# Kernel tuning notes

Measured on AMD Instinct MI355X. Metric: run time of the kernel, lower is better.

The kernel has to match this reference:

```python
import jax, jax.numpy as jnp
import numpy as np

N_NODES = 50000
N_EDGES = 600000
IN_SIZE = 128
HIDDEN = 256
OUT_SIZE = 128


def _xavier(key, shape):
    fan_out, fan_in = shape
    lim = jnp.sqrt(6.0 / (fan_in + fan_out))
    return jax.random.uniform(key, shape, jnp.float32, -lim, lim)


def setup_inputs() -> dict:
    key = jax.random.key(0)
    ks = jax.random.split(key, 8)
    feat = jax.random.normal(ks[0], (N_NODES, IN_SIZE), jnp.float32)
    edge_index = jax.random.randint(ks[1], (2, N_EDGES), 0, N_NODES, jnp.int32)
    return {
        "feat": feat,
        "edge_index": edge_index,
        "W1l": _xavier(ks[2], (HIDDEN, IN_SIZE)),
        "b1": jnp.zeros((HIDDEN,), jnp.float32),
        "W1r": _xavier(ks[3], (HIDDEN, IN_SIZE)),
        "W2l": _xavier(ks[4], (OUT_SIZE, HIDDEN)),
        "b2": jnp.zeros((OUT_SIZE,), jnp.float32),
        "W2r": _xavier(ks[5], (OUT_SIZE, HIDDEN)),
        "Wfc": _xavier(ks[6], (2, OUT_SIZE)),
        "bfc": jnp.zeros((2,), jnp.float32),
    }


def _sage_conv(x, src, dst, Wl, bl, Wr):
    # mean-aggregate neighbor features: messages x[src] scattered to dst
    agg = jax.ops.segment_sum(x[src], dst, num_segments=N_NODES)
    cnt = jax.ops.segment_sum(jnp.ones((src.shape[0],), x.dtype), dst,
                              num_segments=N_NODES)
    agg = agg / jnp.maximum(cnt, 1.0)[:, None]
    out = agg @ Wl.T + bl + x @ Wr.T
    # F.normalize(p=2, dim=-1), eps=1e-12
    norm = jnp.maximum(jnp.linalg.norm(out, axis=-1, keepdims=True), 1e-12)
    return out / norm


def reference(feat, edge_index, W1l, b1, W1r, W2l, b2, W2r, Wfc, bfc):
    src, dst = edge_index[0], edge_index[1]
    h = _sage_conv(feat, src, dst, W1l, b1, W1r)
    h = jax.nn.relu(h)
    h = _sage_conv(h, src, dst, W2l, b2, W2r)
    logits = h @ Wfc.T + bfc
    return jax.nn.softmax(logits, axis=-1)
```

## Files before the change

### kernel.cpp

```cpp
#include <hip/hip_runtime.h>
#include <hip/hip_fp8.h>
#include <math.h>

#define N_NODES  50000
#define N_EDGES  600000
#define CAP      64
#define NB_ZERO  ((N_NODES + 255) / 256)

typedef __attribute__((ext_vector_type(8))) short bf16x8;
typedef __attribute__((ext_vector_type(4))) float f32x4;
typedef unsigned int uint32;

__device__ __forceinline__ unsigned short f2bf(float x) {
  uint32 u = __builtin_bit_cast(uint32, x);
  u += 0x7FFFu + ((u >> 16) & 1u);
  return (unsigned short)(u >> 16);
}
__device__ __forceinline__ float bf2f(uint32 lo16) {
  return __builtin_bit_cast(float, lo16 << 16);
}
__device__ __forceinline__ uint32 pack2(float a, float b) {
  return (uint32)f2bf(a) | ((uint32)f2bf(b) << 16);
}
__device__ __forceinline__ unsigned char f2q(float x) {
  __hip_fp8_e4m3 q(x);
  return __builtin_bit_cast(unsigned char, q);
}
__device__ __forceinline__ float q2f(uint32 b) {
  return (float)__builtin_bit_cast(__hip_fp8_e4m3, (unsigned char)(b & 0xffu));
}

#define PREP_FEAT_BLOCKS 12500
#define PREP_W_BLOCKS    256
__global__ void k_prep(const float* __restrict__ feat, unsigned short* __restrict__ featb,
                       unsigned short* __restrict__ feat8,
                       const float* __restrict__ W1l, const float* __restrict__ W1r,
                       unsigned short* __restrict__ Wc1,
                       const float* __restrict__ W2l, const float* __restrict__ W2r,
                       unsigned short* __restrict__ Wc2,
                       int* __restrict__ cnt) {
  const int bid = blockIdx.x, t = threadIdx.x;
  if (bid < PREP_FEAT_BLOCKS) {
    int i = bid * 256 + t;
    float2 v = ((const float2*)feat)[i];
    ((uint32*)featb)[i] = pack2(v.x, v.y);
    feat8[i] = (unsigned short)f2q(v.x) | ((unsigned short)f2q(v.y) << 8);
  } else if (bid < PREP_FEAT_BLOCKS + PREP_W_BLOCKS) {
    int id = (bid - PREP_FEAT_BLOCKS) * 256 + t;
    int n = id >> 8, k = id & 255;
    float v = (k < 128) ? W1l[n * 128 + k] : W1r[n * 128 + (k - 128)];
    Wc1[id] = f2bf(v);
  } else if (bid < PREP_FEAT_BLOCKS + 2 * PREP_W_BLOCKS) {
    int id = (bid - PREP_FEAT_BLOCKS - PREP_W_BLOCKS) * 256 + t;
    int n = id >> 8, k = id & 255;
    float v = (n < 128) ? W2l[n * 256 + k] : W2r[(n - 128) * 256 + k];
    Wc2[id] = f2bf(v);
  } else {
    int i = (bid - PREP_FEAT_BLOCKS - 2 * PREP_W_BLOCKS) * 256 + t;
    if (i < N_NODES) cnt[i] = 0;
  }
}
#define PREP_BLOCKS (PREP_FEAT_BLOCKS + 2 * PREP_W_BLOCKS + NB_ZERO)

__global__ void k_fill(const int* __restrict__ src, const int* __restrict__ dst,
                       int* __restrict__ cnt, int* __restrict__ col) {
  int i = blockIdx.x * 256 + threadIdx.x;
  if (i < N_EDGES) {
    int d = dst[i];
    int p = atomicAdd(&cnt[d], 1);
    if (p < CAP) col[(size_t)d * CAP + p] = src[i];
  }
}

__device__ __forceinline__ void gather8f8(const uint32* __restrict__ base,
                                          const int* __restrict__ col,
                                          int rs, int dg, int sl, float4& out) {
  int idx[8];
  #pragma unroll
  for (int q = 0; q < 8; ++q) idx[q] = col[rs + q];
  float4 a[8];
  #pragma unroll
  for (int q = 0; q < 8; ++q) a[q] = (float4){0.f, 0.f, 0.f, 0.f};
  int j = 0;
  for (; j + 8 <= dg; j += 8) {
    uint32 v[8];
    #pragma unroll
    for (int q = 0; q < 8; ++q) v[q] = base[(size_t)idx[q] * 32 + sl];
    #pragma unroll
    for (int q = 0; q < 8; ++q) idx[q] = col[rs + j + 8 + q];
    #pragma unroll
    for (int q = 0; q < 8; ++q) {
      a[q].x += q2f(v[q]);
      a[q].y += q2f(v[q] >> 8);
      a[q].z += q2f(v[q] >> 16);
      a[q].w += q2f(v[q] >> 24);
    }
  }
  #pragma unroll
  for (int q = 0; q < 7; ++q) {
    if (j + q < dg) {
      uint32 v = base[(size_t)idx[q] * 32 + sl];
      a[q].x += q2f(v);
      a[q].y += q2f(v >> 8);
      a[q].z += q2f(v >> 16);
      a[q].w += q2f(v >> 24);
    }
  }
  float4 s01, s23, s45, s67, s03, s47;
  s01.x = a[0].x + a[1].x; s01.y = a[0].y + a[1].y; s01.z = a[0].z + a[1].z; s01.w = a[0].w + a[1].w;
  s23.x = a[2].x + a[3].x; s23.y = a[2].y + a[3].y; s23.z = a[2].z + a[3].z; s23.w = a[2].w + a[3].w;
  s45.x = a[4].x + a[5].x; s45.y = a[4].y + a[5].y; s45.z = a[4].z + a[5].z; s45.w = a[4].w + a[5].w;
  s67.x = a[6].x + a[7].x; s67.y = a[6].y + a[7].y; s67.z = a[6].z + a[7].z; s67.w = a[6].w + a[7].w;
  s03.x = s01.x + s23.x; s03.y = s01.y + s23.y; s03.z = s01.z + s23.z; s03.w = s01.w + s23.w;
  s47.x = s45.x + s67.x; s47.y = s45.y + s67.y; s47.z = s45.z + s67.z; s47.w = s45.w + s67.w;
  out.x = s03.x + s47.x; out.y = s03.y + s47.y; out.z = s03.z + s47.z; out.w = s03.w + s47.w;
}

__global__ void k_agg1(const unsigned short* __restrict__ feat8, const int* __restrict__ cnt,
                       const int* __restrict__ col, unsigned short* __restrict__ agg) {
  int lane = threadIdx.x & 63;
  int half = lane >> 5, sl = lane & 31;
  int n = blockIdx.x * 8 + (threadIdx.x >> 6) * 2 + half;
  int dg = min(cnt[n], CAP);
  float4 s;
  gather8f8((const uint32*)feat8, col, n * CAP, dg, sl, s);
  float inv = 1.0f / fmaxf((float)dg, 1.0f);
  uint2 o;
  o.x = pack2(s.x * inv, s.y * inv);
  o.y = pack2(s.z * inv, s.w * inv);
  ((uint2*)agg)[(size_t)n * 32 + sl] = o;
}

__global__ __launch_bounds__(256, 3) void k_gemm1(
    const unsigned short* __restrict__ A0, const unsigned short* __restrict__ A1,
    const unsigned short* __restrict__ W, const float* __restrict__ bias,
    unsigned short* __restrict__ Y) {
  __shared__ unsigned short Ws[2048 * 8];
  __shared__ float red[4][32];
  const int t = threadIdx.x, lane = t & 63, w = t >> 6;
  const int mi = lane & 15, quad = lane >> 4;
  const int rowHalf = w >> 1, colHalf = w & 1;
  const int m0 = blockIdx.x * 64 + rowHalf * 32;
  const int col0 = colHalf * 128;
  const int rowA0 = min(m0 + mi, N_NODES - 1);
  const int rowA1 = min(m0 + 16 + mi, N_NODES - 1);

  f32x4 acc[2][8];
  #pragma unroll
  for (int rt = 0; rt < 2; ++rt)
    #pragma unroll
    for (int nt = 0; nt < 8; ++nt) acc[rt][nt] = (f32x4){0.f, 0.f, 0.f, 0.f};

  #pragma unroll
  for (int ks = 0; ks < 4; ++ks) {
    if (ks) __syncthreads();
    #pragma unroll
    for (int i = 0; i < 8; ++i) {
      int ch0 = (w * 8 + i) * 64;
      int qp = ch0 >> 8, n0 = ch0 & 255;
      const unsigned short* gp = W + (size_t)(n0 + lane) * 256 + ks * 64 + qp * 8;
      unsigned short* lp = Ws + (size_t)ch0 * 8;
      __builtin_amdgcn_global_load_lds(
          (const __attribute__((address_space(1))) void*)gp,
          (__attribute__((address_space(3))) void*)lp, 16, 0, 0);
    }
    const unsigned short* Asrc = (ks < 2) ? A0 : A1;
    const int koff = (ks & 1) * 64;
    bf16x8 af[2][2];
    af[0][0] = *(const bf16x8*)(Asrc + (size_t)rowA0 * 128 + koff + quad * 8);
    af[0][1] = *(const bf16x8*)(Asrc + (size_t)rowA0 * 128 + koff + 32 + quad * 8);
    af[1][0] = *(const bf16x8*)(Asrc + (size_t)rowA1 * 128 + koff + quad * 8);
    af[1][1] = *(const bf16x8*)(Asrc + (size_t)rowA1 * 128 + koff + 32 + quad * 8);
    __syncthreads();
    #pragma unroll
    for (int kc = 0; kc < 2; ++kc)
      #pragma unroll
      for (int nt = 0; nt < 8; ++nt) {
        bf16x8 b = *(const bf16x8*)(Ws + ((size_t)(kc * 4 + quad) * 256 + col0 + nt * 16 + mi) * 8);
        acc[0][nt] = __builtin_amdgcn_mfma_f32_16x16x32_bf16(af[0][kc], b, acc[0][nt], 0, 0, 0);
        acc[1][nt] = __builtin_amdgcn_mfma_f32_16x16x32_bf16(af[1][kc], b, acc[1][nt], 0, 0, 0);
      }
  }

  float ss[2][4] = {};
  #pragma unroll
  for (int nt = 0; nt < 8; ++nt) {
    float bv = bias[col0 + nt * 16 + mi];
    #pragma unroll
    for (int rt = 0; rt < 2; ++rt)
      #pragma unroll
      for (int r = 0; r < 4; ++r) {
        float v = acc[rt][nt][r] + bv;
        acc[rt][nt][r] = v;
        ss[rt][r] += v * v;
      }
  }
  #pragma unroll
  for (int rt = 0; rt < 2; ++rt)
    #pragma unroll
    for (int r = 0; r < 4; ++r) {
      float s = ss[rt][r];
      s += __shfl_xor(s, 1, 64);
      s += __shfl_xor(s, 2, 64);
      s += __shfl_xor(s, 4, 64);
      s += __shfl_xor(s, 8, 64);
      ss[rt][r] = s;
    }
  __syncthreads();
  if (mi == 0) {
    #pragma unroll
    for (int rt = 0; rt < 2; ++rt)
      #pragma unroll
      for (int r = 0; r < 4; ++r)
        red[w][rt * 16 + quad * 4 + r] = ss[rt][r];
  }
  __syncthreads();
  #pragma unroll
  for (int rt = 0; rt < 2; ++rt)
    #pragma unroll
    for (int r = 0; r < 4; ++r) {
      float full = ss[rt][r] + red[w ^ 1][rt * 16 + quad * 4 + r];
      ss[rt][r] = 1.0f / fmaxf(sqrtf(full), 1e-12f);
    }
  #pragma unroll
  for (int rt = 0; rt < 2; ++rt)
    #pragma unroll
    for (int r = 0; r < 4; ++r) {
      int row = m0 + rt * 16 + quad * 4 + r;
      if (row < N_NODES) {
        #pragma unroll
        for (int nt = 0; nt < 8; ++nt)
          Y[(size_t)row * 256 + col0 + nt * 16 + mi] =
              f2bf(fmaxf(acc[rt][nt][r] * ss[rt][r], 0.f));
      }
    }
}

__global__ __launch_bounds__(256, 3) void k_gemm2(
    const unsigned short* __restrict__ A0, const unsigned short* __restrict__ A1,
    const unsigned short* __restrict__ W,
    unsigned char* __restrict__ Tl8, unsigned short* __restrict__ Yr) {
  __shared__ unsigned short Ws[2048 * 8];
  const int t = threadIdx.x, lane = t & 63, w = t >> 6;
  const int mi = lane & 15, quad = lane >> 4;
  const int rb = blockIdx.x >> 1, chh = blockIdx.x & 1;
  const int m0 = rb * 128 + w * 32;
  const int col0 = chh * 128;
  const int rowA0 = min(m0 + mi, N_NODES - 1);
  const int rowA1 = min(m0 + 16 + mi, N_NODES - 1);

  f32x4 acc[2][8];
  #pragma unroll
  for (int rt = 0; rt < 2; ++rt)
    #pragma unroll
    for (int nt = 0; nt < 8; ++nt) acc[rt][nt] = (f32x4){0.f, 0.f, 0.f, 0.f};

  #pragma unroll
  for (int ks = 0; ks < 2; ++ks) {
    if (ks) __syncthreads();
    #pragma unroll
    for (int i = 0; i < 8; ++i) {
      int ch0 = (w * 8 + i) * 64;
      int qp = ch0 >> 7, n0 = ch0 & 127;
      const unsigned short* gp = W + (size_t)(col0 + n0 + lane) * 256 + ks * 128 + qp * 8;
      unsigned short* lp = Ws + (size_t)ch0 * 8;
      __builtin_amdgcn_global_load_lds(
          (const __attribute__((address_space(1))) void*)gp,
          (__attribute__((address_space(3))) void*)lp, 16, 0, 0);
    }
    const unsigned short* Asrc = ks ? A1 : A0;
    bf16x8 af[2][4];
    #pragma unroll
    for (int c = 0; c < 4; ++c) {
      af[0][c] = *(const bf16x8*)(Asrc + (size_t)rowA0 * 256 + c * 32 + quad * 8);
      af[1][c] = *(const bf16x8*)(Asrc + (size_t)rowA1 * 256 + c * 32 + quad * 8);
    }
    __syncthreads();
    #pragma unroll
    for (int c = 0; c < 4; ++c)
      #pragma unroll
      for (int nt = 0; nt < 8; ++nt) {
        bf16x8 b = *(const bf16x8*)(Ws + ((size_t)(c * 4 + quad) * 128 + nt * 16 + mi) * 8);
        acc[0][nt] = __builtin_amdgcn_mfma_f32_16x16x32_bf16(af[0][c], b, acc[0][nt], 0, 0, 0);
        acc[1][nt] = __builtin_amdgcn_mfma_f32_16x16x32_bf16(af[1][c], b, acc[1][nt], 0, 0, 0);
      }
  }

  if (chh == 0) {
    #pragma unroll
    for (int rt = 0; rt < 2; ++rt)
      #pragma unroll
      for (int r = 0; r < 4; ++r) {
        int row = m0 + rt * 16 + quad * 4 + r;
        if (row < N_NODES) {
          #pragma unroll
          for (int nt = 0; nt < 8; ++nt)
            Tl8[(size_t)row * 128 + nt * 16 + mi] = f2q(acc[rt][nt][r]);
        }
      }
  } else {
    #pragma unroll
    for (int rt = 0; rt < 2; ++rt)
      #pragma unroll
      for (int r = 0; r < 4; ++r) {
        int row = m0 + rt * 16 + quad * 4 + r;
        if (row < N_NODES) {
          #pragma unroll
          for (int nt = 0; nt < 8; ++nt)
            Yr[(size_t)row * 128 + nt * 16 + mi] = f2bf(acc[rt][nt][r]);
        }
      }
  }
}

__global__ void k_final(const unsigned char* __restrict__ Tl8, const unsigned short* __restrict__ Tr,
                        const int* __restrict__ cnt, const int* __restrict__ col,
                        const float* __restrict__ b2, const float* __restrict__ Wfc,
                        const float* __restrict__ bfc, float* __restrict__ out) {
  int lane = threadIdx.x & 63;
  int half = lane >> 5, sl = lane & 31;
  int n = blockIdx.x * 8 + (threadIdx.x >> 6) * 2 + half;
  int dg = min(cnt[n], CAP);
  uint2 tv = ((const uint2*)Tr)[(size_t)n * 32 + sl];
  float4 bb = ((const float4*)b2)[sl];
  float4 w0 = ((const float4*)Wfc)[sl];
  float4 w1 = ((const float4*)Wfc)[32 + sl];
  float4 s;
  gather8f8((const uint32*)Tl8, col, n * CAP, dg, sl, s);
  float inv = 1.0f / fmaxf((float)dg, 1.0f);
  float h0 = s.x * inv + bf2f(tv.x & 0xffffu) + bb.x;
  float h1 = s.y * inv + bf2f(tv.x >> 16) + bb.y;
  float h2 = s.z * inv + bf2f(tv.y & 0xffffu) + bb.z;
  float h3 = s.w * inv + bf2f(tv.y >> 16) + bb.w;
  float ss = h0 * h0 + h1 * h1 + h2 * h2 + h3 * h3;
  ss += __shfl_xor(ss, 1, 64);
  ss += __shfl_xor(ss, 2, 64);
  ss += __shfl_xor(ss, 4, 64);
  ss += __shfl_xor(ss, 8, 64);
  ss += __shfl_xor(ss, 16, 64);
  float iv = 1.0f / fmaxf(sqrtf(ss), 1e-12f);
  h0 *= iv; h1 *= iv; h2 *= iv; h3 *= iv;
  float p0 = h0 * w0.x + h1 * w0.y + h2 * w0.z + h3 * w0.w;
  float p1 = h0 * w1.x + h1 * w1.y + h2 * w1.z + h3 * w1.w;
  #pragma unroll
  for (int m = 1; m < 32; m <<= 1) {
    p0 += __shfl_xor(p0, m, 64);
    p1 += __shfl_xor(p1, m, 64);
  }
  if (sl == 0) {
    float l0 = p0 + bfc[0], l1 = p1 + bfc[1];
    float mx = fmaxf(l0, l1);
    float e0 = expf(l0 - mx), e1 = expf(l1 - mx);
    float sden = 1.0f / (e0 + e1);
    out[(size_t)n * 2 + 0] = e0 * sden;
    out[(size_t)n * 2 + 1] = e1 * sden;
  }
}

extern "C" void kernel_launch(void* const* d_in, const int* in_sizes, int n_in,
                              void* d_out, int out_size, void* d_ws, size_t ws_size,
                              hipStream_t stream) {
  const float* feat = (const float*)d_in[0];
  const int* eidx = (const int*)d_in[1];
  const int* src = eidx;
  const int* dst = eidx + N_EDGES;
  const float* W1l = (const float*)d_in[2];
  const float* b1  = (const float*)d_in[3];
  const float* W1r = (const float*)d_in[4];
  const float* W2l = (const float*)d_in[5];
  const float* b2  = (const float*)d_in[6];
  const float* W2r = (const float*)d_in[7];
  const float* Wfc = (const float*)d_in[8];
  const float* bfc = (const float*)d_in[9];
  float* out = (float*)d_out;

  int* cnt       = (int*)d_ws;
  int* col       = cnt + 50176;
  unsigned short* featb = (unsigned short*)(col + 3200064);
  unsigned short* feat8 = featb + 6400000;
  unsigned short* agg1b = feat8 + 3200000;
  unsigned short* h1b   = agg1b + 6400000;
  unsigned char*  Tl8   = (unsigned char*)(h1b + 12800000);
  unsigned short* Trb   = (unsigned short*)(Tl8 + 6400000);
  unsigned short* Wc1   = Trb + 6400000;
  unsigned short* Wc2   = Wc1 + 65536;

  k_prep<<<PREP_BLOCKS, 256, 0, stream>>>(feat, featb, feat8, W1l, W1r, Wc1,
                                          W2l, W2r, Wc2, cnt);
  k_fill<<<(N_EDGES + 255) / 256, 256, 0, stream>>>(src, dst, cnt, col);

  k_agg1<<<N_NODES / 8, 256, 0, stream>>>(feat8, cnt, col, agg1b);
  k_gemm1<<<(N_NODES + 63) / 64, 256, 0, stream>>>(agg1b, featb, Wc1, b1, h1b);
  k_gemm2<<<2 * ((N_NODES + 127) / 128), 256, 0, stream>>>(h1b, h1b + 128, Wc2, Tl8, Trb);
  k_final<<<N_NODES / 8, 256, 0, stream>>>(Tl8, Trb, cnt, col, b2, Wfc, bfc, out);
}
```

Measured before the change: 229.5 us.

## Fuse layer-1 neighbor aggregation into GEMM1 via shared-memory staging

Measured after the change: 251.8 us. 1.1x slower.

```diff
diff --git a/kernel.cpp b/kernel.cpp
--- a/kernel.cpp
+++ b/kernel.cpp
@@ -116,26 +116,13 @@
   out.x = s03.x + s47.x; out.y = s03.y + s47.y; out.z = s03.z + s47.z; out.w = s03.w + s47.w;
 }
 
-__global__ void k_agg1(const unsigned short* __restrict__ feat8, const int* __restrict__ cnt,
-                       const int* __restrict__ col, unsigned short* __restrict__ agg) {
-  int lane = threadIdx.x & 63;
-  int half = lane >> 5, sl = lane & 31;
-  int n = blockIdx.x * 8 + (threadIdx.x >> 6) * 2 + half;
-  int dg = min(cnt[n], CAP);
-  float4 s;
-  gather8f8((const uint32*)feat8, col, n * CAP, dg, sl, s);
-  float inv = 1.0f / fmaxf((float)dg, 1.0f);
-  uint2 o;
-  o.x = pack2(s.x * inv, s.y * inv);
-  o.y = pack2(s.z * inv, s.w * inv);
-  ((uint2*)agg)[(size_t)n * 32 + sl] = o;
-}
-
 __global__ __launch_bounds__(256, 3) void k_gemm1(
-    const unsigned short* __restrict__ A0, const unsigned short* __restrict__ A1,
+    const unsigned short* __restrict__ feat8, const unsigned short* __restrict__ featb,
+    const int* __restrict__ cnt, const int* __restrict__ col,
     const unsigned short* __restrict__ W, const float* __restrict__ bias,
     unsigned short* __restrict__ Y) {
   __shared__ unsigned short Ws[2048 * 8];
+  __shared__ unsigned short aggS[64 * 136];
   __shared__ float red[4][32];
   const int t = threadIdx.x, lane = t & 63, w = t >> 6;
   const int mi = lane & 15, quad = lane >> 4;
@@ -145,6 +132,24 @@
   const int rowA0 = min(m0 + mi, N_NODES - 1);
   const int rowA1 = min(m0 + 16 + mi, N_NODES - 1);
 
+  {
+    const int half = lane >> 5, sl = lane & 31;
+    #pragma unroll
+    for (int p = 0; p < 8; ++p) {
+      int nl = w * 16 + p * 2 + half;
+      int n = min(blockIdx.x * 64 + nl, N_NODES - 1);
+      int dg = min(cnt[n], CAP);
+      float4 s;
+      gather8f8((const uint32*)feat8, col, n * CAP, dg, sl, s);
+      float inv = 1.0f / fmaxf((float)dg, 1.0f);
+      uint2 o;
+      o.x = pack2(s.x * inv, s.y * inv);
+      o.y = pack2(s.z * inv, s.w * inv);
+      ((uint2*)aggS)[nl * 34 + sl] = o;
+    }
+  }
+  __syncthreads();
+
   f32x4 acc[2][8];
   #pragma unroll
   for (int rt = 0; rt < 2; ++rt)
@@ -164,13 +169,20 @@
           (const __attribute__((address_space(1))) void*)gp,
           (__attribute__((address_space(3))) void*)lp, 16, 0, 0);
     }
-    const unsigned short* Asrc = (ks < 2) ? A0 : A1;
     const int koff = (ks & 1) * 64;
     bf16x8 af[2][2];
-    af[0][0] = *(const bf16x8*)(Asrc + (size_t)rowA0 * 128 + koff + quad * 8);
-    af[0][1] = *(const bf16x8*)(Asrc + (size_t)rowA0 * 128 + koff + 32 + quad * 8);
-    af[1][0] = *(const bf16x8*)(Asrc + (size_t)rowA1 * 128 + koff + quad * 8);
-    af[1][1] = *(const bf16x8*)(Asrc + (size_t)rowA1 * 128 + koff + 32 + quad * 8);
+    if (ks < 2) {
+      const int nl0 = rowHalf * 32 + mi, nl1 = rowHalf * 32 + 16 + mi;
+      af[0][0] = *(const bf16x8*)(aggS + nl0 * 136 + koff + quad * 8);
+      af[0][1] = *(const bf16x8*)(aggS + nl0 * 136 + koff + 32 + quad * 8);
+      af[1][0] = *(const bf16x8*)(aggS + nl1 * 136 + koff + quad * 8);
+      af[1][1] = *(const bf16x8*)(aggS + nl1 * 136 + koff + 32 + quad * 8);
+    } else {
+      af[0][0] = *(const bf16x8*)(featb + (size_t)rowA0 * 128 + koff + quad * 8);
+      af[0][1] = *(const bf16x8*)(featb + (size_t)rowA0 * 128 + koff + 32 + quad * 8);
+      af[1][0] = *(const bf16x8*)(featb + (size_t)rowA1 * 128 + koff + quad * 8);
+      af[1][1] = *(const bf16x8*)(featb + (size_t)rowA1 * 128 + koff + 32 + quad * 8);
+    }
     __syncthreads();
     #pragma unroll
     for (int kc = 0; kc < 2; ++kc)
@@ -378,8 +390,7 @@
   int* col       = cnt + 50176;
   unsigned short* featb = (unsigned short*)(col + 3200064);
   unsigned short* feat8 = featb + 6400000;
-  unsigned short* agg1b = feat8 + 3200000;
-  unsigned short* h1b   = agg1b + 6400000;
+  unsigned short* h1b   = feat8 + 3200000;
   unsigned char*  Tl8   = (unsigned char*)(h1b + 12800000);
   unsigned short* Trb   = (unsigned short*)(Tl8 + 6400000);
   unsigned short* Wc1   = Trb + 6400000;
@@ -389,8 +400,7 @@
                                           W2l, W2r, Wc2, cnt);
   k_fill<<<(N_EDGES + 255) / 256, 256, 0, stream>>>(src, dst, cnt, col);
 
-  k_agg1<<<N_NODES / 8, 256, 0, stream>>>(feat8, cnt, col, agg1b);
-  k_gemm1<<<(N_NODES + 63) / 64, 256, 0, stream>>>(agg1b, featb, Wc1, b1, h1b);
+  k_gemm1<<<(N_NODES + 63) / 64, 256, 0, stream>>>(feat8, featb, cnt, col, Wc1, b1, h1b);
   k_gemm2<<<2 * ((N_NODES + 127) / 128), 256, 0, stream>>>(h1b, h1b + 128, Wc2, Tl8, Trb);
   k_final<<<N_NODES / 8, 256, 0, stream>>>(Tl8, Trb, cnt, col, b2, Wfc, bfc, out);
 }
```
